# Kernel optimization log

Measured on AMD Instinct MI355X. Metric: run time of the kernel, lower is better.

The kernel has to match this reference:

```python
import jax, jax.numpy as jnp
import numpy as np

B, S, H, G, W_LOC = 2, 4096, 12, 64, 513  # Longformer-base: window=2*256+1, 64 global slots


def setup_inputs() -> dict:
    key = jax.random.key(0)
    k1, = jax.random.split(key, 1)
    attention_probs = jax.random.uniform(k1, (B, S, H, G + W_LOC), dtype=jnp.float32)
    attention_mask = jnp.zeros((B, S), dtype=jnp.float32)  # all tokens currently kept
    # global tokens are the first G positions of every batch; nonzero(as_tuple) index arrays
    b_idx = jnp.repeat(jnp.arange(B, dtype=jnp.int64), G)
    g_idx = jnp.tile(jnp.arange(G, dtype=jnp.int64), B)
    return {
        "attention_mask": attention_mask,
        "attention_probs": attention_probs,
        "keep_threshold": jnp.asarray(0.005, dtype=jnp.float32),  # base 0.01*6/12 + learned 0
        "max_num_global_attn_indices": G,
        "loc_b": b_idx, "loc_i": g_idx,
        "glob_b": b_idx, "glob_i": g_idx,
    }


def reference(attention_mask, attention_probs, keep_threshold,
              max_num_global_attn_indices, loc_b, loc_i, glob_b, glob_i):
    Gn = max_num_global_attn_indices
    b, s, h, wg = attention_probs.shape
    w = wg - Gn  # local window size, odd
    half = w // 2

    # zero out rows of already-masked tokens (attention_mask < 0)
    probs = jnp.where((attention_mask < 0)[:, :, None, None], 0.0, attention_probs)

    gl = probs[..., :Gn]                              # [B,S,H,G]
    lo = jnp.transpose(probs[..., Gn:], (0, 2, 1, 3))  # [B,H,S,W]

    # anti-diagonal (key-column) sums of the local band; equals the source's
    # conv2d-with-flipped-identity + slice: out[j] = sum_c lo[j + half - c, c]
    lo_p = jnp.pad(lo, ((0, 0), (0, 0), (half, half), (0, 0)))  # [B,H,S+W-1,W]
    rows = jnp.arange(s)[:, None] + (w - 1) - jnp.arange(w)[None, :]  # [S,W]
    diag = lo_p[:, :, rows, jnp.arange(w)[None, :]]  # [B,H,S,W]
    local_sum = diag.sum(axis=(1, 3))                # [B,S] (summed over heads too)

    global_sum = gl.sum(axis=(1, 2))                 # [B,G]
    probs_sum = local_sum.at[loc_b, loc_i].add(global_sum[glob_b, glob_i])

    probs_max = probs_sum.max(axis=-1, keepdims=True)
    scores = probs_sum / probs_max

    thr = jnp.maximum(jnp.float32(1e-5), jnp.asarray(keep_threshold, jnp.float32).reshape(()))
    new_attention_mask = jnp.where(scores < thr, jnp.float32(-10000.0), jnp.float32(0.0))
    return new_attention_mask, scores
```

## Files before the change

kernel.cpp:

```cpp
#include <hip/hip_runtime.h>
#include <float.h>

#define Bsz 2
#define Ssz 4096
#define Hsz 12
#define Gsz 64
#define Wsz 513
#define Csz (Gsz + Wsz)
#define ROW (Hsz * Csz)
#define HALF 256
#define RPB 8
#define WIN (RPB + Wsz - 1)

#define PSUM_SZ ((size_t)Bsz * Ssz)
#define GACC_SZ ((size_t)Bsz * Gsz)

__global__ __launch_bounds__(256) void k1_fused(
    const float* __restrict__ probs, const float* __restrict__ mask,
    float* __restrict__ psum, float* __restrict__ gacc)
{
    __shared__ float lds[ROW];
    __shared__ float win[WIN];
    const int t = threadIdx.x;
    const int row0 = blockIdx.x * RPB;
    const int b = row0 / Ssz;
    float g = 0.f;

    for (int w = t; w < WIN; w += 256) win[w] = 0.f;

    for (int r = 0; r < RPB; ++r) {
        const int row = row0 + r;
        const float4* src = (const float4*)(probs + (size_t)row * ROW);
        float4* dst = (float4*)lds;
        #pragma unroll
        for (int idx = t; idx < ROW / 4; idx += 256) dst[idx] = src[idx];
        __syncthreads();

        const float scale = (mask[row] < 0.f) ? 0.f : 1.f;
        for (int c = t; c < Csz; c += 256) {
            float v = 0.f;
            #pragma unroll
            for (int h = 0; h < Hsz; ++h) v += lds[h * Csz + c];
            v *= scale;
            if (c < Gsz) g += v;
            else win[r + (c - Gsz)] += v;
        }
        __syncthreads();
    }

    const int i_base = (row0 - b * Ssz) - HALF;
    for (int w = t; w < WIN; w += 256) {
        const int i = i_base + w;
        if (i >= 0 && i < Ssz) atomicAdd(&psum[b * Ssz + i], win[w]);
    }
    if (t < Gsz) atomicAdd(&gacc[b * Gsz + t], g);
}

__global__ void k3_scatter(const int* __restrict__ loc_b, const int* __restrict__ loc_i,
                           const int* __restrict__ glob_b, const int* __restrict__ glob_i,
                           const float* __restrict__ gacc, float* __restrict__ psum, int n)
{
    int k = blockIdx.x * blockDim.x + threadIdx.x;
    if (k < n)
        atomicAdd(&psum[loc_b[k] * Ssz + loc_i[k]], gacc[glob_b[k] * Gsz + glob_i[k]]);
}

__global__ __launch_bounds__(1024) void k4_final(
    const float* __restrict__ psum, const float* __restrict__ thr_p,
    float* __restrict__ out)
{
    const int b = blockIdx.x;
    const int t = threadIdx.x;
    const float* p = psum + (size_t)b * Ssz;

    float m = -FLT_MAX;
    for (int i = t; i < Ssz; i += 1024) m = fmaxf(m, p[i]);
    #pragma unroll
    for (int off = 32; off >= 1; off >>= 1) m = fmaxf(m, __shfl_down(m, off, 64));

    __shared__ float red[16];
    const int wave = t >> 6, lane = t & 63;
    if (lane == 0) red[wave] = m;
    __syncthreads();
    if (t == 0) {
        float mm = red[0];
        #pragma unroll
        for (int w = 1; w < 16; ++w) mm = fmaxf(mm, red[w]);
        red[0] = mm;
    }
    __syncthreads();
    const float mx = red[0];
    const float thr = fmaxf(1e-5f, thr_p[0]);

    for (int i = t; i < Ssz; i += 1024) {
        float sc = p[i] / mx;
        out[(size_t)Bsz * Ssz + (size_t)b * Ssz + i] = sc;
        out[(size_t)b * Ssz + i] = (sc < thr) ? -10000.f : 0.f;
    }
}

extern "C" void kernel_launch(void* const* d_in, const int* in_sizes, int n_in,
                              void* d_out, int out_size, void* d_ws, size_t ws_size,
                              hipStream_t stream)
{
    const float* mask  = (const float*)d_in[0];
    const float* probs = (const float*)d_in[1];
    const float* thr   = (const float*)d_in[2];
    const int* loc_b  = (const int*)d_in[4];
    const int* loc_i  = (const int*)d_in[5];
    const int* glob_b = (const int*)d_in[6];
    const int* glob_i = (const int*)d_in[7];
    const int n_idx = in_sizes[4];

    float* psum = (float*)d_ws;
    float* gacc = psum + PSUM_SZ;
    float* out  = (float*)d_out;

    hipMemsetAsync(psum, 0, (PSUM_SZ + GACC_SZ) * sizeof(float), stream);

    k1_fused<<<dim3(Bsz * Ssz / RPB), dim3(256), 0, stream>>>(probs, mask, psum, gacc);
    k3_scatter<<<dim3(1), dim3(128), 0, stream>>>(loc_b, loc_i, glob_b, glob_i, gacc, psum, n_idx);
    k4_final<<<dim3(Bsz), dim3(1024), 0, stream>>>(psum, thr, out);
}
```

Baseline: 332.6 us.

## Read probs directly from global with LDS window atomics; fuse scatter into final

The reduction kernel no longer stages each row through a large LDS buffer with per-row barriers. Each thread now reads its column for all 8 rows straight from global memory and accumulates window sums with LDS atomics. This cuts LDS use and removes the per-row synchronisation, so more loads can be in flight and occupancy can rise. The global-token scatter is folded into the final kernel, which copies psum into LDS and applies the scatter there, removing one kernel launch. The trade-off is scalar rather than float4 loads and LDS atomic traffic.

```diff
diff --git a/kernel.cpp b/kernel.cpp
--- a/kernel.cpp
+++ b/kernel.cpp
@@ -19,34 +19,35 @@
     const float* __restrict__ probs, const float* __restrict__ mask,
     float* __restrict__ psum, float* __restrict__ gacc)
 {
-    __shared__ float lds[ROW];
     __shared__ float win[WIN];
     const int t = threadIdx.x;
     const int row0 = blockIdx.x * RPB;
     const int b = row0 / Ssz;
+
+    for (int w = t; w < WIN; w += 256) win[w] = 0.f;
+    __syncthreads();
+
+    float scale[RPB];
+    #pragma unroll
+    for (int r = 0; r < RPB; ++r)
+        scale[r] = (mask[row0 + r] < 0.f) ? 0.f : 1.f;
+
+    const float* base = probs + (size_t)row0 * ROW;
     float g = 0.f;
 
-    for (int w = t; w < WIN; w += 256) win[w] = 0.f;
-
-    for (int r = 0; r < RPB; ++r) {
-        const int row = row0 + r;
-        const float4* src = (const float4*)(probs + (size_t)row * ROW);
-        float4* dst = (float4*)lds;
+    for (int c = t; c < Csz; c += 256) {
         #pragma unroll
-        for (int idx = t; idx < ROW / 4; idx += 256) dst[idx] = src[idx];
-        __syncthreads();
-
-        const float scale = (mask[row] < 0.f) ? 0.f : 1.f;
-        for (int c = t; c < Csz; c += 256) {
+        for (int r = 0; r < RPB; ++r) {
             float v = 0.f;
             #pragma unroll
-            for (int h = 0; h < Hsz; ++h) v += lds[h * Csz + c];
-            v *= scale;
+            for (int h = 0; h < Hsz; ++h)
+                v += base[(size_t)r * ROW + h * Csz + c];
+            v *= scale[r];
             if (c < Gsz) g += v;
-            else win[r + (c - Gsz)] += v;
+            else atomicAdd(&win[r + (c - Gsz)], v);
         }
-        __syncthreads();
     }
+    __syncthreads();
 
     const int i_base = (row0 - b * Ssz) - HALF;
     for (int w = t; w < WIN; w += 256) {
@@ -56,29 +57,31 @@
     if (t < Gsz) atomicAdd(&gacc[b * Gsz + t], g);
 }
 
-__global__ void k3_scatter(const int* __restrict__ loc_b, const int* __restrict__ loc_i,
-                           const int* __restrict__ glob_b, const int* __restrict__ glob_i,
-                           const float* __restrict__ gacc, float* __restrict__ psum, int n)
+__global__ __launch_bounds__(1024) void k4_final(
+    const float* __restrict__ psum, const float* __restrict__ gacc,
+    const float* __restrict__ thr_p,
+    const int* __restrict__ loc_b, const int* __restrict__ loc_i,
+    const int* __restrict__ glob_b, const int* __restrict__ glob_i,
+    int n_idx, float* __restrict__ out)
 {
-    int k = blockIdx.x * blockDim.x + threadIdx.x;
-    if (k < n)
-        atomicAdd(&psum[loc_b[k] * Ssz + loc_i[k]], gacc[glob_b[k] * Gsz + glob_i[k]]);
-}
-
-__global__ __launch_bounds__(1024) void k4_final(
-    const float* __restrict__ psum, const float* __restrict__ thr_p,
-    float* __restrict__ out)
-{
+    __shared__ float p_lds[Ssz];
+    __shared__ float red[16];
     const int b = blockIdx.x;
     const int t = threadIdx.x;
     const float* p = psum + (size_t)b * Ssz;
 
+    for (int i = t; i < Ssz; i += 1024) p_lds[i] = p[i];
+    __syncthreads();
+
+    if (t < n_idx && loc_b[t] == b)
+        atomicAdd(&p_lds[loc_i[t]], gacc[glob_b[t] * Gsz + glob_i[t]]);
+    __syncthreads();
+
     float m = -FLT_MAX;
-    for (int i = t; i < Ssz; i += 1024) m = fmaxf(m, p[i]);
+    for (int i = t; i < Ssz; i += 1024) m = fmaxf(m, p_lds[i]);
     #pragma unroll
     for (int off = 32; off >= 1; off >>= 1) m = fmaxf(m, __shfl_down(m, off, 64));
 
-    __shared__ float red[16];
     const int wave = t >> 6, lane = t & 63;
     if (lane == 0) red[wave] = m;
     __syncthreads();
@@ -93,7 +96,7 @@
     const float thr = fmaxf(1e-5f, thr_p[0]);
 
     for (int i = t; i < Ssz; i += 1024) {
-        float sc = p[i] / mx;
+        float sc = p_lds[i] / mx;
         out[(size_t)Bsz * Ssz + (size_t)b * Ssz + i] = sc;
         out[(size_t)b * Ssz + i] = (sc < thr) ? -10000.f : 0.f;
     }
@@ -119,6 +122,7 @@
     hipMemsetAsync(psum, 0, (PSUM_SZ + GACC_SZ) * sizeof(float), stream);
 
     k1_fused<<<dim3(Bsz * Ssz / RPB), dim3(256), 0, stream>>>(probs, mask, psum, gacc);
-    k3_scatter<<<dim3(1), dim3(128), 0, stream>>>(loc_b, loc_i, glob_b, glob_i, gacc, psum, n_idx);
-    k4_final<<<dim3(Bsz), dim3(1024), 0, stream>>>(psum, thr, out);
+    k4_final<<<dim3(Bsz), dim3(1024), 0, stream>>>(psum, gacc, thr,
+                                                   loc_b, loc_i, glob_b, glob_i,
+                                                   n_idx, out);
 }
```

After: 340.6 us. +2.4%, slower.
